# Optimization experiments

Hardware: AMD Instinct MI355X
Metric: run time of the kernel (lower is better)

Reference implementation:

```python
import jax, jax.numpy as jnp
import numpy as np

N_ATOMS = 50000
N_INT = 800000  # interactions (i,j pairs)
N_IN = 128
NFM = 128
LOG2 = float(np.log(2.0))


def ssp(a):
    # shifted softplus: log(0.5*exp(x) + 0.5) = softplus(x) - log(2)
    return jax.nn.softplus(a) - LOG2


def setup_inputs() -> dict:
    key = jax.random.key(0)
    ks = jax.random.split(key, 12)
    s = 1.0 / np.sqrt(NFM)
    inp = {
        "x": jax.random.normal(ks[0], (N_ATOMS, NFM), dtype=jnp.float32),
        "dijk": jax.random.normal(ks[1], (N_INT, N_IN), dtype=jnp.float32),
        "idx_j": jax.random.randint(ks[2], (N_INT,), 0, N_ATOMS),
        "seg_i": jnp.sort(jax.random.randint(ks[3], (N_INT,), 0, N_ATOMS)),
        "seg_j": jnp.arange(N_INT),
        "seg_i_sum": jnp.ones((N_ATOMS,), dtype=jnp.int64 if jax.config.jax_enable_x64 else jnp.int32),
        # filternet params
        "W_f1": jax.random.normal(ks[4], (N_IN, NFM), dtype=jnp.float32) * s,
        "b_f1": jnp.zeros((NFM,), dtype=jnp.float32),
        "W_f2": jax.random.normal(ks[5], (NFM, NFM), dtype=jnp.float32) * s,
        "b_f2": jnp.zeros((NFM,), dtype=jnp.float32),
        # cfconv params
        "W_in2fac": jax.random.normal(ks[6], (NFM, NFM), dtype=jnp.float32) * s,
        "W_fac2out": jax.random.normal(ks[7], (NFM, NFM), dtype=jnp.float32) * s,
        "b_fac2out": jnp.zeros((NFM,), dtype=jnp.float32),
        # output dense params
        "W_dense": jax.random.normal(ks[8], (NFM, NFM), dtype=jnp.float32) * s,
        "b_dense": jnp.zeros((NFM,), dtype=jnp.float32),
    }
    return inp


def reference(x, dijk, idx_j, seg_i, seg_j, seg_i_sum,
              W_f1, b_f1, W_f2, b_f2,
              W_in2fac, W_fac2out, b_fac2out,
              W_dense, b_dense):
    n_atoms = x.shape[0]
    n_int = idx_j.shape[0]
    # CFnetFilter: two shifted-softplus dense layers over triples, pool -> per-interaction filters
    h = ssp(dijk @ W_f1 + b_f1)                                   # [T, nFM]
    w_ijk = ssp(h @ W_f2 + b_f2)                                  # [T, nFM]
    w_ij = jax.ops.segment_sum(w_ijk, seg_j, num_segments=n_int)  # [E, nFM]
    # CFConv: in2fac dense, gather neighbor features, filter-multiply, segment-sum pool, fac2out dense
    f = x @ W_in2fac                                              # [N, nFM]
    f_j = f[idx_j]                                                # gather -> [E, nFM]
    wf = w_ij * f_j                                               # [E, nFM]
    conv = jax.ops.segment_sum(wf, seg_i, num_segments=n_atoms)   # [N, nFM]
    c = ssp(conv @ W_fac2out + b_fac2out)                         # [N, nFM]
    # output dense (no activation) + residual
    v = c @ W_dense + b_dense                                     # [N, nFM]
    y = x + v
    return (y, v)
```

## Files before the change

### kernel.cpp

```cpp
#include <hip/hip_runtime.h>
#include <hip/hip_bf16.h>
#include <stdint.h>

#define NATOMS 50000
#define NINT   800000
#define NFM    128
#define VOFF   (NATOMS*NFM)

typedef __bf16 bf16x8 __attribute__((ext_vector_type(8)));
typedef float  f32x4  __attribute__((ext_vector_type(4)));
typedef unsigned short u16;
typedef u16 u16x8 __attribute__((ext_vector_type(8)));

__device__ __forceinline__ u16 f2b(float f){
  uint32_t u = __float_as_uint(f);
  u += 0x7fffu + ((u >> 16) & 1u);
  return (u16)(u >> 16);
}
__device__ __forceinline__ float b2f(u16 b){ return __uint_as_float(((uint32_t)b) << 16); }

__device__ __forceinline__ float sspf(float x){
  float t = exp2f(-fabsf(x) * 1.44269504088896f);
  return fmaxf(x, 0.0f) + 0.69314718055995f * log2f(1.0f + t) - 0.69314718055995f;
}

__global__ void prep_weights_k(const float* __restrict__ w0, const float* __restrict__ w1,
                               const float* __restrict__ w2, const float* __restrict__ w3,
                               const float* __restrict__ w4, u16* __restrict__ wt){
  const float* srcs[5] = {w0, w1, w2, w3, w4};
  const float* src = srcs[blockIdx.x];
  u16* dst = wt + (size_t)blockIdx.x * NFM * NFM;
  for (int i = threadIdx.x; i < NFM*NFM; i += blockDim.x){
    int n = i >> 7, k = i & 127;
    dst[i] = f2b(src[k*NFM + n]);
  }
}

__device__ __forceinline__ void stage_inp(u16* lsA, const float* __restrict__ src,
                                          int base_row, int n_total, int t){
  #pragma unroll
  for (int pp = 0; pp < 8; ++pp){
    int id  = pp*512 + t;
    int row = id >> 4, c = id & 15;
    int grow = base_row + row;
    float4 v0 = make_float4(0.f,0.f,0.f,0.f), v1 = v0;
    if (grow < n_total){
      const float4* gp = reinterpret_cast<const float4*>(src + (size_t)grow*NFM + c*8);
      v0 = gp[0]; v1 = gp[1];
    }
    u16x8 pk;
    pk[0]=f2b(v0.x); pk[1]=f2b(v0.y); pk[2]=f2b(v0.z); pk[3]=f2b(v0.w);
    pk[4]=f2b(v1.x); pk[5]=f2b(v1.y); pk[6]=f2b(v1.z); pk[7]=f2b(v1.w);
    int byte = row*256 + ((c*16) ^ ((row & 7) << 4));
    *reinterpret_cast<u16x8*>(reinterpret_cast<char*>(lsA) + byte) = pk;
  }
}

__device__ __forceinline__ void stage_w(u16* lsW, const u16* __restrict__ wt, int t){
  #pragma unroll
  for (int pp = 0; pp < 4; ++pp){
    int id = pp*512 + t;
    int n = id >> 4, c = id & 15;
    u16x8 v = *reinterpret_cast<const u16x8*>(wt + n*NFM + c*8);
    int byte = n*256 + ((c*16) ^ ((n & 7) << 4));
    *reinterpret_cast<u16x8*>(reinterpret_cast<char*>(lsW) + byte) = v;
  }
}

__device__ __forceinline__ void gemm_tile(const u16* lsA, const u16* lsW,
                                          int wrow, int l15, int lk, f32x4 acc[2][8]){
  #pragma unroll
  for (int ks = 0; ks < 4; ++ks){
    int kb2 = (ks*32 + lk*8) * 2;
    int r0 = wrow + l15, r1 = wrow + 16 + l15;
    bf16x8 a0 = *reinterpret_cast<const bf16x8*>(reinterpret_cast<const char*>(lsA) + r0*256 + (kb2 ^ ((r0 & 7) << 4)));
    bf16x8 a1 = *reinterpret_cast<const bf16x8*>(reinterpret_cast<const char*>(lsA) + r1*256 + (kb2 ^ ((r1 & 7) << 4)));
    #pragma unroll
    for (int ni = 0; ni < 8; ++ni){
      int n = ni*16 + l15;
      bf16x8 b = *reinterpret_cast<const bf16x8*>(reinterpret_cast<const char*>(lsW) + n*256 + (kb2 ^ ((n & 7) << 4)));
      acc[0][ni] = __builtin_amdgcn_mfma_f32_16x16x32_bf16(a0, b, acc[0][ni], 0, 0, 0);
      acc[1][ni] = __builtin_amdgcn_mfma_f32_16x16x32_bf16(a1, b, acc[1][ni], 0, 0, 0);
    }
  }
}

__global__ __launch_bounds__(512, 2) void in2fac_k(const float* __restrict__ x,
                                                   const u16* __restrict__ wt,
                                                   u16* __restrict__ f_g){
  __shared__ u16 lsA[256*128];
  __shared__ u16 lsW[128*128];
  int t = threadIdx.x;
  int B0 = blockIdx.x * 256;
  stage_inp(lsA, x, B0, NATOMS, t);
  stage_w(lsW, wt, t);
  __syncthreads();
  int wid = t >> 6, lane = t & 63, l15 = lane & 15, lk = lane >> 4;
  int wrow = wid * 32;
  f32x4 acc[2][8] = {};
  gemm_tile(lsA, lsW, wrow, l15, lk, acc);
  #pragma unroll
  for (int mi = 0; mi < 2; ++mi)
    #pragma unroll
    for (int ni = 0; ni < 8; ++ni)
      #pragma unroll
      for (int j = 0; j < 4; ++j){
        int grow = B0 + wrow + mi*16 + lk*4 + j;
        if (grow < NATOMS) f_g[(size_t)grow*NFM + ni*16 + l15] = f2b(acc[mi][ni][j]);
      }
}

__global__ __launch_bounds__(512) __attribute__((amdgpu_waves_per_eu(4, 4)))
void cfnet_inter_k(
    const float* __restrict__ dijk, const int* __restrict__ idx_j, const int* __restrict__ seg_i,
    const float* __restrict__ b_f1, const float* __restrict__ b_f2,
    const u16* __restrict__ wt1, const u16* __restrict__ wt2,
    const u16* __restrict__ f_g, float* __restrict__ conv){
  __shared__ u16 lsW[128*128];
  __shared__ u16 lsBuf[256*64];
  __shared__ int lsSeg[256];
  __shared__ int lsIdx[256];
  int t = threadIdx.x;
  int B0 = blockIdx.x * 256;
  int wid = t >> 6, lane = t & 63, l15 = lane & 15, lk = lane >> 4;

  if (t < 256){ lsSeg[t] = seg_i[B0 + t]; lsIdx[t] = idx_j[B0 + t]; }
  stage_w(lsW, wt1, t);

  float bias1[8];
  #pragma unroll
  for (int ni = 0; ni < 8; ++ni) bias1[ni] = b_f1[ni*16 + l15];

  __syncthreads();

  char* wbase = reinterpret_cast<char*>(lsBuf) + wid*4096;
  bf16x8 h[2][4];
  #pragma unroll
  for (int mi = 0; mi < 2; ++mi){
    bf16x8 a[4];
    const float* abase = dijk + (size_t)(B0 + wid*32 + mi*16 + l15) * NFM;
    #pragma unroll
    for (int ks = 0; ks < 4; ++ks){
      const float4* gp = reinterpret_cast<const float4*>(abase + ks*32 + lk*8);
      float4 v0 = gp[0], v1 = gp[1];
      u16x8 pk;
      pk[0]=f2b(v0.x); pk[1]=f2b(v0.y); pk[2]=f2b(v0.z); pk[3]=f2b(v0.w);
      pk[4]=f2b(v1.x); pk[5]=f2b(v1.y); pk[6]=f2b(v1.z); pk[7]=f2b(v1.w);
      a[ks] = *reinterpret_cast<bf16x8*>(&pk);
    }
    f32x4 acc[8] = {};
    #pragma unroll
    for (int ks = 0; ks < 4; ++ks){
      int kb2 = (ks*32 + lk*8) * 2;
      #pragma unroll
      for (int ni = 0; ni < 8; ++ni){
        int n = ni*16 + l15;
        bf16x8 b = *reinterpret_cast<const bf16x8*>(reinterpret_cast<const char*>(lsW) + n*256 + (kb2 ^ ((n & 7) << 4)));
        acc[ni] = __builtin_amdgcn_mfma_f32_16x16x32_bf16(a[ks], b, acc[ni], 0, 0, 0);
      }
    }
    #pragma unroll
    for (int ni = 0; ni < 8; ++ni){
      int col = ni*16 + l15;
      #pragma unroll
      for (int j = 0; j < 4; ++j){
        int r = lk*4 + j;
        *reinterpret_cast<u16*>(wbase + r*256 + ((col*2) ^ ((r & 7) << 4))) = f2b(sspf(acc[ni][j] + bias1[ni]));
      }
    }
    #pragma unroll
    for (int ks = 0; ks < 4; ++ks){
      h[mi][ks] = *reinterpret_cast<const bf16x8*>(wbase + l15*256 + (((ks*32 + lk*8)*2) ^ ((l15 & 7) << 4)));
    }
  }

  float bias2[8];
  #pragma unroll
  for (int ni = 0; ni < 8; ++ni) bias2[ni] = b_f2[ni*16 + l15];

  __syncthreads();
  stage_w(lsW, wt2, t);
  __syncthreads();

  int cR = t & 63, q = t >> 6;
  int qs = q*32, qe = qs + 32;
  #pragma unroll
  for (int p = 0; p < 2; ++p){
    f32x4 acc[2][4] = {};
    #pragma unroll
    for (int ks = 0; ks < 4; ++ks){
      int kb2 = (ks*32 + lk*8) * 2;
      #pragma unroll
      for (int nn = 0; nn < 4; ++nn){
        int n = (p*4 + nn)*16 + l15;
        bf16x8 b = *reinterpret_cast<const bf16x8*>(reinterpret_cast<const char*>(lsW) + n*256 + (kb2 ^ ((n & 7) << 4)));
        acc[0][nn] = __builtin_amdgcn_mfma_f32_16x16x32_bf16(h[0][ks], b, acc[0][nn], 0, 0, 0);
        acc[1][nn] = __builtin_amdgcn_mfma_f32_16x16x32_bf16(h[1][ks], b, acc[1][nn], 0, 0, 0);
      }
    }
    #pragma unroll
    for (int mi = 0; mi < 2; ++mi)
      #pragma unroll
      for (int nn = 0; nn < 4; ++nn){
        int ch = nn*16 + l15;
        #pragma unroll
        for (int j = 0; j < 4; ++j){
          int r = wid*32 + mi*16 + lk*4 + j;
          *reinterpret_cast<u16*>(reinterpret_cast<char*>(lsBuf) + r*128 + ((ch*2) ^ ((r & 7) << 4))) = f2b(sspf(acc[mi][nn][j] + bias2[p*4+nn]));
        }
      }
    __syncthreads();
    {
      int gcol = p*64 + cR;
      int prevseg = (qs > 0) ? lsSeg[qs-1] : (B0 > 0 ? seg_i[B0-1] : -1);
      int nextseg = (qe < 256) ? lsSeg[qe] : (B0 + 256 < NINT ? seg_i[B0+256] : -1);
      float wsum = 0.f;
      int cur = lsSeg[qs], rs = qs;
      #pragma unroll 8
      for (int r = qs; r < qe; ++r){
        int s = lsSeg[r];
        float fv = b2f(f_g[(size_t)lsIdx[r]*NFM + gcol]);
        float wv = b2f(*reinterpret_cast<const u16*>(reinterpret_cast<const char*>(lsBuf) + r*128 + ((cR*2) ^ ((r & 7) << 4))));
        if (s != cur){
          float* dp = conv + (size_t)cur*NFM + gcol;
          if (rs == qs && prevseg == cur) atomicAdd(dp, wsum); else *dp = wsum;
          cur = s; rs = r; wsum = 0.f;
        }
        wsum = fmaf(wv, fv, wsum);
      }
      float* dp = conv + (size_t)cur*NFM + gcol;
      if ((rs == qs && prevseg == cur) || nextseg == cur) atomicAdd(dp, wsum); else *dp = wsum;
    }
    __syncthreads();
  }
}

__global__ __launch_bounds__(512, 2) void out_k(const float* __restrict__ conv,
    const float* __restrict__ x, const u16* __restrict__ wt3, const u16* __restrict__ wt4,
    const float* __restrict__ b3, const float* __restrict__ b4, float* __restrict__ out){
  __shared__ u16 lsA[256*128];
  __shared__ u16 lsW1[128*128];
  __shared__ u16 lsW2[128*128];
  int t = threadIdx.x;
  int B0 = blockIdx.x * 256;
  stage_inp(lsA, conv, B0, NATOMS, t);
  stage_w(lsW1, wt3, t);
  stage_w(lsW2, wt4, t);
  __syncthreads();
  int wid = t >> 6, lane = t & 63, l15 = lane & 15, lk = lane >> 4;
  int wrow = wid * 32;
  float bias3[8], bias4[8];
  #pragma unroll
  for (int ni = 0; ni < 8; ++ni){ bias3[ni] = b3[ni*16 + l15]; bias4[ni] = b4[ni*16 + l15]; }

  f32x4 acc1[2][8] = {};
  gemm_tile(lsA, lsW1, wrow, l15, lk, acc1);
  #pragma unroll
  for (int mi = 0; mi < 2; ++mi)
    #pragma unroll
    for (int ni = 0; ni < 8; ++ni)
      #pragma unroll
      for (int j = 0; j < 4; ++j){
        int row = wrow + mi*16 + lk*4 + j;
        int col = ni*16 + l15;
        u16 hb = f2b(sspf(acc1[mi][ni][j] + bias3[ni]));
        int byte = row*256 + ((col*2) ^ ((row & 7) << 4));
        *reinterpret_cast<u16*>(reinterpret_cast<char*>(lsA) + byte) = hb;
      }

  f32x4 acc2[2][8] = {};
  gemm_tile(lsA, lsW2, wrow, l15, lk, acc2);
  #pragma unroll
  for (int mi = 0; mi < 2; ++mi)
    #pragma unroll
    for (int ni = 0; ni < 8; ++ni)
      #pragma unroll
      for (int j = 0; j < 4; ++j){
        int grow = B0 + wrow + mi*16 + lk*4 + j;
        if (grow < NATOMS){
          int col = ni*16 + l15;
          float v = acc2[mi][ni][j] + bias4[ni];
          float yv = x[(size_t)grow*NFM + col] + v;
          out[(size_t)grow*NFM + col] = yv;
          out[(size_t)VOFF + (size_t)grow*NFM + col] = v;
        }
      }
}

extern "C" void kernel_launch(void* const* d_in, const int* in_sizes, int n_in,
                              void* d_out, int out_size, void* d_ws, size_t ws_size,
                              hipStream_t stream){
  const float* x        = (const float*)d_in[0];
  const float* dijk     = (const float*)d_in[1];
  const int*   idx_j    = (const int*)d_in[2];
  const int*   seg_i    = (const int*)d_in[3];
  const float* W_f1     = (const float*)d_in[6];
  const float* b_f1     = (const float*)d_in[7];
  const float* W_f2     = (const float*)d_in[8];
  const float* b_f2     = (const float*)d_in[9];
  const float* W_in2fac = (const float*)d_in[10];
  const float* W_fac2o  = (const float*)d_in[11];
  const float* b_fac2o  = (const float*)d_in[12];
  const float* W_dense  = (const float*)d_in[13];
  const float* b_dense  = (const float*)d_in[14];
  float* out = (float*)d_out;

  char* ws = (char*)d_ws;
  u16*   f_g  = (u16*)ws;
  float* conv = (float*)(ws + 12800000);
  u16*   wt   = (u16*)(ws + 38400000);
  u16* wt1 = wt;
  u16* wt2 = wt + 16384;
  u16* wt5 = wt + 2*16384;
  u16* wt3 = wt + 3*16384;
  u16* wt4 = wt + 4*16384;

  prep_weights_k<<<5, 256, 0, stream>>>(W_f1, W_f2, W_in2fac, W_fac2o, W_dense, wt);
  hipMemsetAsync(conv, 0, (size_t)NATOMS*NFM*sizeof(float), stream);
  in2fac_k<<<(NATOMS + 255)/256, 512, 0, stream>>>(x, wt5, f_g);
  cfnet_inter_k<<<NINT/256, 512, 0, stream>>>(dijk, idx_j, seg_i, b_f1, b_f2, wt1, wt2, f_g, conv);
  out_k<<<(NATOMS + 255)/256, 512, 0, stream>>>(conv, x, wt3, wt4, b_fac2o, b_dense, out);
}
```

Before: 367.9 us.

## Shrink LDS buffer and split filter GEMMs into narrower passes for higher occupancy

```diff
diff --git a/kernel.cpp b/kernel.cpp
--- a/kernel.cpp
+++ b/kernel.cpp
@@ -11,6 +11,7 @@
 typedef float  f32x4  __attribute__((ext_vector_type(4)));
 typedef unsigned short u16;
 typedef u16 u16x8 __attribute__((ext_vector_type(8)));
+typedef u16 u16x4 __attribute__((ext_vector_type(4)));
 
 __device__ __forceinline__ u16 f2b(float f){
   uint32_t u = __float_as_uint(f);
@@ -110,14 +111,14 @@
       }
 }
 
-__global__ __launch_bounds__(512) __attribute__((amdgpu_waves_per_eu(4, 4)))
+__global__ __launch_bounds__(512) __attribute__((amdgpu_waves_per_eu(6, 8)))
 void cfnet_inter_k(
     const float* __restrict__ dijk, const int* __restrict__ idx_j, const int* __restrict__ seg_i,
     const float* __restrict__ b_f1, const float* __restrict__ b_f2,
     const u16* __restrict__ wt1, const u16* __restrict__ wt2,
     const u16* __restrict__ f_g, float* __restrict__ conv){
   __shared__ u16 lsW[128*128];
-  __shared__ u16 lsBuf[256*64];
+  __shared__ u16 lsBuf[8192];
   __shared__ int lsSeg[256];
   __shared__ int lsIdx[256];
   int t = threadIdx.x;
@@ -133,7 +134,7 @@
 
   __syncthreads();
 
-  char* wbase = reinterpret_cast<char*>(lsBuf) + wid*4096;
+  char* wbase = reinterpret_cast<char*>(lsBuf) + wid*2048;
   bf16x8 h[2][4];
   #pragma unroll
   for (int mi = 0; mi < 2; ++mi){
@@ -148,85 +149,94 @@
       pk[4]=f2b(v1.x); pk[5]=f2b(v1.y); pk[6]=f2b(v1.z); pk[7]=f2b(v1.w);
       a[ks] = *reinterpret_cast<bf16x8*>(&pk);
     }
-    f32x4 acc[8] = {};
+    #pragma unroll
+    for (int p = 0; p < 2; ++p){
+      f32x4 acc[4] = {};
+      #pragma unroll
+      for (int ks = 0; ks < 4; ++ks){
+        int kb2 = (ks*32 + lk*8) * 2;
+        #pragma unroll
+        for (int nn = 0; nn < 4; ++nn){
+          int n = (p*4 + nn)*16 + l15;
+          bf16x8 b = *reinterpret_cast<const bf16x8*>(reinterpret_cast<const char*>(lsW) + n*256 + (kb2 ^ ((n & 7) << 4)));
+          acc[nn] = __builtin_amdgcn_mfma_f32_16x16x32_bf16(a[ks], b, acc[nn], 0, 0, 0);
+        }
+      }
+      #pragma unroll
+      for (int nn = 0; nn < 4; ++nn){
+        int col = nn*16 + l15;
+        #pragma unroll
+        for (int j = 0; j < 4; ++j){
+          int r = lk*4 + j;
+          *reinterpret_cast<u16*>(wbase + r*128 + ((col*2) ^ ((r & 7) << 4))) = f2b(sspf(acc[nn][j] + bias1[p*4+nn]));
+        }
+      }
+      #pragma unroll
+      for (int ksl = 0; ksl < 2; ++ksl)
+        h[mi][p*2+ksl] = *reinterpret_cast<const bf16x8*>(wbase + l15*128 + ((ksl*64 + lk*16) ^ ((l15 & 7) << 4)));
+    }
+  }
+
+  __syncthreads();
+  stage_w(lsW, wt2, t);
+  __syncthreads();
+
+  char* sbase = reinterpret_cast<char*>(lsBuf);
+  int cR = t & 31, qch = t >> 5;
+  int qs = qch*16, qe = qs + 16;
+  #pragma unroll
+  for (int p4 = 0; p4 < 4; ++p4){
+    f32x4 acc[2][2] = {};
     #pragma unroll
     for (int ks = 0; ks < 4; ++ks){
       int kb2 = (ks*32 + lk*8) * 2;
       #pragma unroll
-      for (int ni = 0; ni < 8; ++ni){
-        int n = ni*16 + l15;
-        bf16x8 b = *reinterpret_cast<const bf16x8*>(reinterpret_cast<const char*>(lsW) + n*256 + (kb2 ^ ((n & 7) << 4)));
-        acc[ni] = __builtin_amdgcn_mfma_f32_16x16x32_bf16(a[ks], b, acc[ni], 0, 0, 0);
-      }
-    }
-    #pragma unroll
-    for (int ni = 0; ni < 8; ++ni){
-      int col = ni*16 + l15;
-      #pragma unroll
-      for (int j = 0; j < 4; ++j){
-        int r = lk*4 + j;
-        *reinterpret_cast<u16*>(wbase + r*256 + ((col*2) ^ ((r & 7) << 4))) = f2b(sspf(acc[ni][j] + bias1[ni]));
-      }
-    }
-    #pragma unroll
-    for (int ks = 0; ks < 4; ++ks){
-      h[mi][ks] = *reinterpret_cast<const bf16x8*>(wbase + l15*256 + (((ks*32 + lk*8)*2) ^ ((l15 & 7) << 4)));
-    }
-  }
-
-  float bias2[8];
-  #pragma unroll
-  for (int ni = 0; ni < 8; ++ni) bias2[ni] = b_f2[ni*16 + l15];
-
-  __syncthreads();
-  stage_w(lsW, wt2, t);
-  __syncthreads();
-
-  int cR = t & 63, q = t >> 6;
-  int qs = q*32, qe = qs + 32;
-  #pragma unroll
-  for (int p = 0; p < 2; ++p){
-    f32x4 acc[2][4] = {};
-    #pragma unroll
-    for (int ks = 0; ks < 4; ++ks){
-      int kb2 = (ks*32 + lk*8) * 2;
-      #pragma unroll
-      for (int nn = 0; nn < 4; ++nn){
-        int n = (p*4 + nn)*16 + l15;
+      for (int nn = 0; nn < 2; ++nn){
+        int n = (p4*2 + nn)*16 + l15;
         bf16x8 b = *reinterpret_cast<const bf16x8*>(reinterpret_cast<const char*>(lsW) + n*256 + (kb2 ^ ((n & 7) << 4)));
         acc[0][nn] = __builtin_amdgcn_mfma_f32_16x16x32_bf16(h[0][ks], b, acc[0][nn], 0, 0, 0);
         acc[1][nn] = __builtin_amdgcn_mfma_f32_16x16x32_bf16(h[1][ks], b, acc[1][nn], 0, 0, 0);
       }
     }
+    float bb0 = b_f2[(p4*2)*16 + l15];
+    float bb1 = b_f2[(p4*2+1)*16 + l15];
     #pragma unroll
     for (int mi = 0; mi < 2; ++mi)
       #pragma unroll
-      for (int nn = 0; nn < 4; ++nn){
-        int ch = nn*16 + l15;
-        #pragma unroll
-        for (int j = 0; j < 4; ++j){
-          int r = wid*32 + mi*16 + lk*4 + j;
-          *reinterpret_cast<u16*>(reinterpret_cast<char*>(lsBuf) + r*128 + ((ch*2) ^ ((r & 7) << 4))) = f2b(sspf(acc[mi][nn][j] + bias2[p*4+nn]));
-        }
+      for (int nn = 0; nn < 2; ++nn){
+        float bb = nn ? bb1 : bb0;
+        int c = nn*16 + l15;
+        int r0 = wid*32 + mi*16 + lk*4;
+        u16x4 qq;
+        qq[0] = f2b(sspf(acc[mi][nn][0] + bb));
+        qq[1] = f2b(sspf(acc[mi][nn][1] + bb));
+        qq[2] = f2b(sspf(acc[mi][nn][2] + bb));
+        qq[3] = f2b(sspf(acc[mi][nn][3] + bb));
+        *reinterpret_cast<u16x4*>(sbase + c*512 + ((r0*2) ^ ((c & 15) << 4))) = qq;
       }
     __syncthreads();
     {
-      int gcol = p*64 + cR;
+      int gcol = p4*32 + cR;
       int prevseg = (qs > 0) ? lsSeg[qs-1] : (B0 > 0 ? seg_i[B0-1] : -1);
       int nextseg = (qe < 256) ? lsSeg[qe] : (B0 + 256 < NINT ? seg_i[B0+256] : -1);
       float wsum = 0.f;
       int cur = lsSeg[qs], rs = qs;
-      #pragma unroll 8
-      for (int r = qs; r < qe; ++r){
-        int s = lsSeg[r];
-        float fv = b2f(f_g[(size_t)lsIdx[r]*NFM + gcol]);
-        float wv = b2f(*reinterpret_cast<const u16*>(reinterpret_cast<const char*>(lsBuf) + r*128 + ((cR*2) ^ ((r & 7) << 4))));
-        if (s != cur){
-          float* dp = conv + (size_t)cur*NFM + gcol;
-          if (rs == qs && prevseg == cur) atomicAdd(dp, wsum); else *dp = wsum;
-          cur = s; rs = r; wsum = 0.f;
+      #pragma unroll
+      for (int i8 = 0; i8 < 2; ++i8){
+        u16x8 wv = *reinterpret_cast<const u16x8*>(sbase + cR*512 + (((qs + i8*8)*2) ^ ((cR & 15) << 4)));
+        #pragma unroll
+        for (int o = 0; o < 8; ++o){
+          int r = qs + i8*8 + o;
+          int s = lsSeg[r];
+          float fv = b2f(f_g[(size_t)lsIdx[r]*NFM + gcol]);
+          float wvv = b2f(wv[o]);
+          if (s != cur){
+            float* dp = conv + (size_t)cur*NFM + gcol;
+            if (rs == qs && prevseg == cur) atomicAdd(dp, wsum); else *dp = wsum;
+            cur = s; rs = r; wsum = 0.f;
+          }
+          wsum = fmaf(wvv, fv, wsum);
         }
-        wsum = fmaf(wv, fv, wsum);
       }
       float* dp = conv + (size_t)cur*NFM + gcol;
       if ((rs == qs && prevseg == cur) || nextseg == cur) atomicAdd(dp, wsum); else *dp = wsum;
```

Measured after the change: 435.5 us. 18.4% more time.

## Split fused filter/conv kernel into chunked filter and gather-scatter kernels

Applied to the files above, without the earlier changes.

```diff
diff --git a/kernel.cpp b/kernel.cpp
--- a/kernel.cpp
+++ b/kernel.cpp
@@ -6,18 +6,23 @@
 #define NINT   800000
 #define NFM    128
 #define VOFF   (NATOMS*NFM)
+#define C0BLK  1563
+#define C1BLK  1562
+#define C1ROW  (C0BLK*256)
 
 typedef __bf16 bf16x8 __attribute__((ext_vector_type(8)));
 typedef float  f32x4  __attribute__((ext_vector_type(4)));
 typedef unsigned short u16;
 typedef u16 u16x8 __attribute__((ext_vector_type(8)));
+typedef u16 u16x4 __attribute__((ext_vector_type(4)));
 
 __device__ __forceinline__ u16 f2b(float f){
-  uint32_t u = __float_as_uint(f);
-  u += 0x7fffu + ((u >> 16) & 1u);
-  return (u16)(u >> 16);
-}
-__device__ __forceinline__ float b2f(u16 b){ return __uint_as_float(((uint32_t)b) << 16); }
+  __bf16 h = (__bf16)f;
+  return __builtin_bit_cast(u16, h);
+}
+__device__ __forceinline__ float b2f(u16 v){
+  return (float)__builtin_bit_cast(__bf16, v);
+}
 
 __device__ __forceinline__ float sspf(float x){
   float t = exp2f(-fabsf(x) * 1.44269504088896f);
@@ -111,128 +116,142 @@
 }
 
 __global__ __launch_bounds__(512) __attribute__((amdgpu_waves_per_eu(4, 4)))
-void cfnet_inter_k(
-    const float* __restrict__ dijk, const int* __restrict__ idx_j, const int* __restrict__ seg_i,
-    const float* __restrict__ b_f1, const float* __restrict__ b_f2,
-    const u16* __restrict__ wt1, const u16* __restrict__ wt2,
-    const u16* __restrict__ f_g, float* __restrict__ conv){
-  __shared__ u16 lsW[128*128];
-  __shared__ u16 lsBuf[256*64];
+void filter_k(const float* __restrict__ dijk,
+              const float* __restrict__ b_f1, const float* __restrict__ b_f2,
+              const u16* __restrict__ wt1, const u16* __restrict__ wt2,
+              u16* __restrict__ w_g, int C0){
+  __shared__ u16 lsW[2*128*128];
+  __shared__ u16 lsS[8192];
+  int t = threadIdx.x;
+  int B0 = C0 + blockIdx.x * 256;
+  int wid = t >> 6, lane = t & 63, l15 = lane & 15, lk = lane >> 4;
+
+  stage_w(lsW, wt1, t);
+  stage_w(lsW + 16384, wt2, t);
+
+  float bias1[8], bias2[8];
+  #pragma unroll
+  for (int ni = 0; ni < 8; ++ni){ bias1[ni] = b_f1[ni*16 + l15]; bias2[ni] = b_f2[ni*16 + l15]; }
+
+  __syncthreads();
+
+  char* wbase = reinterpret_cast<char*>(lsS) + wid*2048;
+  const char* lsW1b = reinterpret_cast<const char*>(lsW);
+  const char* lsW2b = reinterpret_cast<const char*>(lsW + 16384);
+
+  #pragma unroll
+  for (int mi = 0; mi < 2; ++mi){
+    bf16x8 a[4];
+    {
+      const float* abase = dijk + (size_t)(B0 + wid*32 + mi*16 + l15) * NFM;
+      float4 raw[8];
+      #pragma unroll
+      for (int ks = 0; ks < 4; ++ks){
+        const float4* gp = reinterpret_cast<const float4*>(abase + ks*32 + lk*8);
+        raw[ks*2] = gp[0]; raw[ks*2+1] = gp[1];
+      }
+      #pragma unroll
+      for (int ks = 0; ks < 4; ++ks){
+        float4 v0 = raw[ks*2], v1 = raw[ks*2+1];
+        u16x8 pk;
+        pk[0]=f2b(v0.x); pk[1]=f2b(v0.y); pk[2]=f2b(v0.z); pk[3]=f2b(v0.w);
+        pk[4]=f2b(v1.x); pk[5]=f2b(v1.y); pk[6]=f2b(v1.z); pk[7]=f2b(v1.w);
+        a[ks] = __builtin_bit_cast(bf16x8, pk);
+      }
+    }
+    f32x4 acc[8] = {};
+    #pragma unroll
+    for (int ks = 0; ks < 4; ++ks){
+      int kb2 = (ks*32 + lk*8) * 2;
+      #pragma unroll
+      for (int ni = 0; ni < 8; ++ni){
+        int n = ni*16 + l15;
+        bf16x8 b = *reinterpret_cast<const bf16x8*>(lsW1b + n*256 + (kb2 ^ ((n & 7) << 4)));
+        acc[ni] = __builtin_amdgcn_mfma_f32_16x16x32_bf16(a[ks], b, acc[ni], 0, 0, 0);
+      }
+    }
+    bf16x8 h[4];
+    #pragma unroll
+    for (int p = 0; p < 2; ++p){
+      #pragma unroll
+      for (int nn = 0; nn < 4; ++nn){
+        int col = nn*16 + l15;
+        #pragma unroll
+        for (int j = 0; j < 4; ++j){
+          int r = lk*4 + j;
+          *reinterpret_cast<u16*>(wbase + r*128 + ((col*2) ^ ((r & 7) << 4))) = f2b(sspf(acc[p*4+nn][j] + bias1[p*4+nn]));
+        }
+      }
+      #pragma unroll
+      for (int ksl = 0; ksl < 2; ++ksl)
+        h[p*2+ksl] = *reinterpret_cast<const bf16x8*>(wbase + l15*128 + ((ksl*64 + lk*16) ^ ((l15 & 7) << 4)));
+    }
+    #pragma unroll
+    for (int p = 0; p < 2; ++p){
+      f32x4 acc2[4] = {};
+      #pragma unroll
+      for (int ks = 0; ks < 4; ++ks){
+        int kb2 = (ks*32 + lk*8) * 2;
+        #pragma unroll
+        for (int nn = 0; nn < 4; ++nn){
+          int n = (p*4 + nn)*16 + l15;
+          bf16x8 b = *reinterpret_cast<const bf16x8*>(lsW2b + n*256 + (kb2 ^ ((n & 7) << 4)));
+          acc2[nn] = __builtin_amdgcn_mfma_f32_16x16x32_bf16(h[ks], b, acc2[nn], 0, 0, 0);
+        }
+      }
+      #pragma unroll
+      for (int nn = 0; nn < 4; ++nn){
+        int col = nn*16 + l15;
+        #pragma unroll
+        for (int j = 0; j < 4; ++j){
+          int r = lk*4 + j;
+          *reinterpret_cast<u16*>(wbase + r*128 + ((col*2) ^ ((r & 7) << 4))) = f2b(sspf(acc2[nn][j] + bias2[p*4+nn]));
+        }
+      }
+      int row16 = lane & 15, chunk = lane >> 4;
+      u16x8 v0 = *reinterpret_cast<const u16x8*>(wbase + row16*128 + ((chunk*32) ^ ((row16 & 7) << 4)));
+      u16x8 v1 = *reinterpret_cast<const u16x8*>(wbase + row16*128 + ((chunk*32 + 16) ^ ((row16 & 7) << 4)));
+      u16* gdst = w_g + (size_t)(blockIdx.x*256 + wid*32 + mi*16 + row16)*NFM + p*64 + chunk*16;
+      *reinterpret_cast<u16x8*>(gdst)     = v0;
+      *reinterpret_cast<u16x8*>(gdst + 8) = v1;
+    }
+  }
+}
+
+__global__ __launch_bounds__(512) void conv_k(const int* __restrict__ idx_j,
+    const int* __restrict__ seg_i, const u16* __restrict__ f_g,
+    const u16* __restrict__ w_g, float* __restrict__ conv, int C0){
   __shared__ int lsSeg[256];
   __shared__ int lsIdx[256];
   int t = threadIdx.x;
-  int B0 = blockIdx.x * 256;
-  int wid = t >> 6, lane = t & 63, l15 = lane & 15, lk = lane >> 4;
-
+  int B0 = C0 + blockIdx.x * 256;
   if (t < 256){ lsSeg[t] = seg_i[B0 + t]; lsIdx[t] = idx_j[B0 + t]; }
-  stage_w(lsW, wt1, t);
-
-  float bias1[8];
-  #pragma unroll
-  for (int ni = 0; ni < 8; ++ni) bias1[ni] = b_f1[ni*16 + l15];
-
   __syncthreads();
-
-  char* wbase = reinterpret_cast<char*>(lsBuf) + wid*4096;
-  bf16x8 h[2][4];
-  #pragma unroll
-  for (int mi = 0; mi < 2; ++mi){
-    bf16x8 a[4];
-    const float* abase = dijk + (size_t)(B0 + wid*32 + mi*16 + l15) * NFM;
-    #pragma unroll
-    for (int ks = 0; ks < 4; ++ks){
-      const float4* gp = reinterpret_cast<const float4*>(abase + ks*32 + lk*8);
-      float4 v0 = gp[0], v1 = gp[1];
-      u16x8 pk;
-      pk[0]=f2b(v0.x); pk[1]=f2b(v0.y); pk[2]=f2b(v0.z); pk[3]=f2b(v0.w);
-      pk[4]=f2b(v1.x); pk[5]=f2b(v1.y); pk[6]=f2b(v1.z); pk[7]=f2b(v1.w);
-      a[ks] = *reinterpret_cast<bf16x8*>(&pk);
-    }
-    f32x4 acc[8] = {};
-    #pragma unroll
-    for (int ks = 0; ks < 4; ++ks){
-      int kb2 = (ks*32 + lk*8) * 2;
-      #pragma unroll
-      for (int ni = 0; ni < 8; ++ni){
-        int n = ni*16 + l15;
-        bf16x8 b = *reinterpret_cast<const bf16x8*>(reinterpret_cast<const char*>(lsW) + n*256 + (kb2 ^ ((n & 7) << 4)));
-        acc[ni] = __builtin_amdgcn_mfma_f32_16x16x32_bf16(a[ks], b, acc[ni], 0, 0, 0);
-      }
-    }
-    #pragma unroll
-    for (int ni = 0; ni < 8; ++ni){
-      int col = ni*16 + l15;
-      #pragma unroll
-      for (int j = 0; j < 4; ++j){
-        int r = lk*4 + j;
-        *reinterpret_cast<u16*>(wbase + r*256 + ((col*2) ^ ((r & 7) << 4))) = f2b(sspf(acc[ni][j] + bias1[ni]));
-      }
-    }
-    #pragma unroll
-    for (int ks = 0; ks < 4; ++ks){
-      h[mi][ks] = *reinterpret_cast<const bf16x8*>(wbase + l15*256 + (((ks*32 + lk*8)*2) ^ ((l15 & 7) << 4)));
-    }
-  }
-
-  float bias2[8];
-  #pragma unroll
-  for (int ni = 0; ni < 8; ++ni) bias2[ni] = b_f2[ni*16 + l15];
-
-  __syncthreads();
-  stage_w(lsW, wt2, t);
-  __syncthreads();
-
-  int cR = t & 63, q = t >> 6;
+  int c2 = t & 63, q = t >> 6;
   int qs = q*32, qe = qs + 32;
-  #pragma unroll
-  for (int p = 0; p < 2; ++p){
-    f32x4 acc[2][4] = {};
-    #pragma unroll
-    for (int ks = 0; ks < 4; ++ks){
-      int kb2 = (ks*32 + lk*8) * 2;
-      #pragma unroll
-      for (int nn = 0; nn < 4; ++nn){
-        int n = (p*4 + nn)*16 + l15;
-        bf16x8 b = *reinterpret_cast<const bf16x8*>(reinterpret_cast<const char*>(lsW) + n*256 + (kb2 ^ ((n & 7) << 4)));
-        acc[0][nn] = __builtin_amdgcn_mfma_f32_16x16x32_bf16(h[0][ks], b, acc[0][nn], 0, 0, 0);
-        acc[1][nn] = __builtin_amdgcn_mfma_f32_16x16x32_bf16(h[1][ks], b, acc[1][nn], 0, 0, 0);
-      }
-    }
-    #pragma unroll
-    for (int mi = 0; mi < 2; ++mi)
-      #pragma unroll
-      for (int nn = 0; nn < 4; ++nn){
-        int ch = nn*16 + l15;
-        #pragma unroll
-        for (int j = 0; j < 4; ++j){
-          int r = wid*32 + mi*16 + lk*4 + j;
-          *reinterpret_cast<u16*>(reinterpret_cast<char*>(lsBuf) + r*128 + ((ch*2) ^ ((r & 7) << 4))) = f2b(sspf(acc[mi][nn][j] + bias2[p*4+nn]));
-        }
-      }
-    __syncthreads();
-    {
-      int gcol = p*64 + cR;
-      int prevseg = (qs > 0) ? lsSeg[qs-1] : (B0 > 0 ? seg_i[B0-1] : -1);
-      int nextseg = (qe < 256) ? lsSeg[qe] : (B0 + 256 < NINT ? seg_i[B0+256] : -1);
-      float wsum = 0.f;
-      int cur = lsSeg[qs], rs = qs;
-      #pragma unroll 8
-      for (int r = qs; r < qe; ++r){
-        int s = lsSeg[r];
-        float fv = b2f(f_g[(size_t)lsIdx[r]*NFM + gcol]);
-        float wv = b2f(*reinterpret_cast<const u16*>(reinterpret_cast<const char*>(lsBuf) + r*128 + ((cR*2) ^ ((r & 7) << 4))));
-        if (s != cur){
-          float* dp = conv + (size_t)cur*NFM + gcol;
-          if (rs == qs && prevseg == cur) atomicAdd(dp, wsum); else *dp = wsum;
-          cur = s; rs = r; wsum = 0.f;
-        }
-        wsum = fmaf(wv, fv, wsum);
-      }
-      float* dp = conv + (size_t)cur*NFM + gcol;
-      if ((rs == qs && prevseg == cur) || nextseg == cur) atomicAdd(dp, wsum); else *dp = wsum;
-    }
-    __syncthreads();
-  }
+  int gc = c2*2;
+  int prevseg = (qs > 0) ? lsSeg[qs-1] : (B0 > 0 ? seg_i[B0-1] : -1);
+  int nextseg = (qe < 256) ? lsSeg[qe] : (B0 + 256 < NINT ? seg_i[B0+256] : -1);
+  const u16* wtile = w_g + (size_t)blockIdx.x*256*NFM;
+  float s0 = 0.f, s1 = 0.f;
+  int cur = lsSeg[qs], rs = qs;
+  #pragma unroll 8
+  for (int r = qs; r < qe; ++r){
+    int sg = lsSeg[r];
+    uint32_t wv = *reinterpret_cast<const uint32_t*>(wtile + (size_t)r*NFM + gc);
+    uint32_t fv = *reinterpret_cast<const uint32_t*>(f_g + (size_t)lsIdx[r]*NFM + gc);
+    if (sg != cur){
+      float* dp = conv + (size_t)cur*NFM + gc;
+      if (rs == qs && prevseg == cur){ atomicAdd(dp, s0); atomicAdd(dp+1, s1); }
+      else { *reinterpret_cast<float2*>(dp) = make_float2(s0, s1); }
+      cur = sg; rs = r; s0 = 0.f; s1 = 0.f;
+    }
+    s0 = fmaf(b2f((u16)(wv & 0xffff)), b2f((u16)(fv & 0xffff)), s0);
+    s1 = fmaf(b2f((u16)(wv >> 16)),   b2f((u16)(fv >> 16)),   s1);
+  }
+  float* dp = conv + (size_t)cur*NFM + gc;
+  if ((rs == qs && prevseg == cur) || nextseg == cur){ atomicAdd(dp, s0); atomicAdd(dp+1, s1); }
+  else { *reinterpret_cast<float2*>(dp) = make_float2(s0, s1); }
 }
 
 __global__ __launch_bounds__(512, 2) void out_k(const float* __restrict__ conv,
@@ -309,6 +328,7 @@
   u16*   f_g  = (u16*)ws;
   float* conv = (float*)(ws + 12800000);
   u16*   wt   = (u16*)(ws + 38400000);
+  u16*   w_g  = (u16*)(ws + 38600000);
   u16* wt1 = wt;
   u16* wt2 = wt + 16384;
   u16* wt5 = wt + 2*16384;
@@ -318,6 +338,9 @@
   prep_weights_k<<<5, 256, 0, stream>>>(W_f1, W_f2, W_in2fac, W_fac2o, W_dense, wt);
   hipMemsetAsync(conv, 0, (size_t)NATOMS*NFM*sizeof(float), stream);
   in2fac_k<<<(NATOMS + 255)/256, 512, 0, stream>>>(x, wt5, f_g);
-  cfnet_inter_k<<<NINT/256, 512, 0, stream>>>(dijk, idx_j, seg_i, b_f1, b_f2, wt1, wt2, f_g, conv);
+  filter_k<<<C0BLK, 512, 0, stream>>>(dijk, b_f1, b_f2, wt1, wt2, w_g, 0);
+  conv_k<<<C0BLK, 512, 0, stream>>>(idx_j, seg_i, f_g, w_g, conv, 0);
+  filter_k<<<C1BLK, 512, 0, stream>>>(dijk, b_f1, b_f2, wt1, wt2, w_g, C1ROW);
+  conv_k<<<C1BLK, 512, 0, stream>>>(idx_j, seg_i, f_g, w_g, conv, C1ROW);
   out_k<<<(NATOMS + 255)/256, 512, 0, stream>>>(conv, x, wt3, wt4, b_fac2o, b_dense, out);
 }
```

Result: faster. 350.5 us (-4.7%).
